# Kernel tuning notes

Hardware: AMD Instinct MI355X
Metric: run time of the kernel (lower is better)

Reference implementation:

```python
import jax, jax.numpy as jnp
import numpy as np

B, S, E, H = 8, 2048, 1024, 128  # batch, seq, emd_dim, head_size
DROP_P = 0.1


def setup_inputs() -> dict:
    key = jax.random.key(0)
    kx, ku, kq, kk, kv = jax.random.split(key, 5)
    x = jax.random.normal(kx, (B, S, E), dtype=jnp.float32)
    drop_u = jax.random.uniform(ku, (B, S, S), dtype=jnp.float32)
    # Linear(emd_dim, head_size, bias=False): store weights as [E, H] so y = x @ W
    scale = 1.0 / np.sqrt(E)
    wq = jax.random.uniform(kq, (E, H), dtype=jnp.float32, minval=-scale, maxval=scale)
    wk = jax.random.uniform(kk, (E, H), dtype=jnp.float32, minval=-scale, maxval=scale)
    wv = jax.random.uniform(kv, (E, H), dtype=jnp.float32, minval=-scale, maxval=scale)
    return {"x": x, "wq": wq, "wk": wk, "wv": wv, "drop_u": drop_u}


def reference(x, wq, wk, wv, drop_u):
    Edim = x.shape[-1]
    q = x @ wq  # [B,S,H]
    k = x @ wk
    v = x @ wv
    # NOTE: module scales by emd_dim**-0.5 (E), not head_size**-0.5
    att = jnp.einsum("bsh,bth->bst", q, k) * (Edim ** -0.5)
    att = jax.nn.softmax(att, axis=-1)
    # deterministic inverted dropout with p=0.1
    keep = (drop_u >= DROP_P).astype(att.dtype) / (1.0 - DROP_P)
    att = att * keep
    return jnp.einsum("bst,bth->bsh", att, v)
```

## Files before the change

### kernel.cpp

```cpp
#include <hip/hip_runtime.h>
#include <hip/hip_bf16.h>
#include <stdint.h>
#include <stddef.h>

#define B_ 8
#define S_ 2048
#define E_ 1024
#define H_ 128
#define NR_ (B_ * S_)

typedef __attribute__((ext_vector_type(8))) short short8;
typedef __attribute__((ext_vector_type(4))) short short4v;
typedef __attribute__((ext_vector_type(4))) float f32x4;

__device__ __forceinline__ short f2bf(float f){
  uint32_t u = __builtin_bit_cast(uint32_t, f);
  u = (u + 0x7FFFu + ((u >> 16) & 1u)) >> 16;
  return (short)(uint16_t)u;
}

__device__ __forceinline__ short8 pack8(f32x4 a, f32x4 b){
  union { short8 s; uint32_t u[4]; } r;
  asm("v_cvt_pk_bf16_f32 %0, %1, %2" : "=v"(r.u[0]) : "v"(a[0]), "v"(a[1]));
  asm("v_cvt_pk_bf16_f32 %0, %1, %2" : "=v"(r.u[1]) : "v"(a[2]), "v"(a[3]));
  asm("v_cvt_pk_bf16_f32 %0, %1, %2" : "=v"(r.u[2]) : "v"(b[0]), "v"(b[1]));
  asm("v_cvt_pk_bf16_f32 %0, %1, %2" : "=v"(r.u[3]) : "v"(b[2]), "v"(b[3]));
  return r.s;
}

#define GLOBAL_AS __attribute__((address_space(1)))
#define LDS_AS    __attribute__((address_space(3)))
__device__ __forceinline__ void async16(const void* g, void* l){
  __builtin_amdgcn_global_load_lds((const GLOBAL_AS uint32_t*)g,
                                   (LDS_AS uint32_t*)l, 16, 0, 0);
}

__global__ void prep(const float* __restrict__ wq, const float* __restrict__ wk,
                     const float* __restrict__ wv, short* __restrict__ wt){
  __shared__ float t[32][33];
  int idx = blockIdx.x;
  int hb  = idx & 3;
  int eb  = (idx >> 2) & 31;
  int w   = idx >> 7;
  const float* src = (w == 0) ? wq : (w == 1) ? wk : wv;
  int c  = threadIdx.x & 31;
  int r0 = threadIdx.x >> 5;
#pragma unroll
  for (int i = 0; i < 4; i++){
    int r = r0 * 4 + i;
    t[r][c] = src[(size_t)(eb * 32 + r) * H_ + hb * 32 + c];
  }
  __syncthreads();
#pragma unroll
  for (int i = 0; i < 4; i++){
    int r = r0 * 4 + i;
    wt[(size_t)(w * 128 + hb * 32 + r) * E_ + eb * 32 + c] = f2bf(t[c][r]);
  }
}

__launch_bounds__(256)
__global__ void qkv_gemm(const float* __restrict__ x, const short* __restrict__ wt,
                         short* __restrict__ qm, short* __restrict__ km,
                         short* __restrict__ vt){
  __shared__ __align__(16) short smem[16896];
  const int wave = threadIdx.x >> 6;
  const int lane = threadIdx.x & 63;
  const int l16  = lane & 15;
  const int quad = lane >> 4;
  const int nb   = blockIdx.x;
  const int m0   = blockIdx.y * 128;
  const int n0   = nb * 128;

  f32x4 acc[4][4];
#pragma unroll
  for (int i = 0; i < 4; i++)
#pragma unroll
    for (int j = 0; j < 4; j++) acc[i][j] = (f32x4)(0.0f);

  int cA[2], rA[2], qA[2];
#pragma unroll
  for (int i = 0; i < 2; i++){
    cA[i] = wave * 2 + i;
    rA[i] = cA[i] * 16 + (lane >> 2);
    qA[i] = ((lane & 3) ^ ((rA[i] >> 1) & 3)) & 3;
  }

  f32x4 a0[2], a1[2];

#define A_LOAD(k0)                                                            \
  {                                                                           \
    _Pragma("unroll")                                                         \
    for (int i = 0; i < 2; i++){                                              \
      const float* s_ = x + (size_t)(m0 + rA[i]) * E_ + (k0) + qA[i] * 8;     \
      a0[i] = *(const f32x4*)s_;                                              \
      a1[i] = *(const f32x4*)(s_ + 4);                                        \
    }                                                                         \
  }

#define A_WRITE(buf)                                                          \
  {                                                                           \
    _Pragma("unroll")                                                         \
    for (int i = 0; i < 2; i++)                                               \
      *(short8*)((char*)(smem + (buf) * 4096) + cA[i] * 1024 + lane * 16) =   \
          pack8(a0[i], a1[i]);                                                \
  }

#define B_STAGE(buf, k0)                                                      \
  {                                                                           \
    _Pragma("unroll")                                                         \
    for (int i = 0; i < 2; i++){                                              \
      int c = wave * 2 + i;                                                   \
      int r = c * 16 + (lane >> 2);                                           \
      int q = ((lane & 3) ^ ((r >> 1) & 3)) & 3;                              \
      async16(wt + (size_t)(n0 + r) * E_ + (k0) + q * 8,                      \
              (char*)(smem + 8192 + (buf) * 4096) + c * 1024);                \
    }                                                                         \
  }

  A_LOAD(0)
  B_STAGE(0, 0)
  A_WRITE(0)
  for (int ks = 0; ks < 32; ks++){
    const int k0 = ks * 32;
    __syncthreads();
    if (ks < 31){
      A_LOAD(k0 + 32)
      B_STAGE((ks + 1) & 1, k0 + 32)
    }

    const short* a = smem + (ks & 1) * 4096;
    const short* b = smem + 8192 + (ks & 1) * 4096;
    short8 af[4], bf[4];
#pragma unroll
    for (int t = 0; t < 4; t++){
      int ra = (wave & 1) * 64 + t * 16 + l16;
      int pa = (quad ^ ((ra >> 1) & 3)) & 3;
      af[t] = *(const short8*)(a + ra * 32 + pa * 8);
      int rb = (wave >> 1) * 64 + t * 16 + l16;
      int pb = (quad ^ ((rb >> 1) & 3)) & 3;
      bf[t] = *(const short8*)(b + rb * 32 + pb * 8);
    }
#pragma unroll
    for (int mt = 0; mt < 4; mt++)
#pragma unroll
      for (int nt = 0; nt < 4; nt++)
        acc[mt][nt] = __builtin_amdgcn_mfma_f32_16x16x32_bf16(af[mt], bf[nt], acc[mt][nt], 0, 0, 0);

    if (ks < 31){
      A_WRITE((ks + 1) & 1)
    }
  }
#undef A_LOAD
#undef A_WRITE
#undef B_STAGE

  if (nb != 2){
    short* dst = (nb == 0) ? qm : km;
#pragma unroll
    for (int mt = 0; mt < 4; mt++)
#pragma unroll
      for (int nt = 0; nt < 4; nt++){
        int row = m0 + (wave & 1) * 64 + mt * 16 + quad * 4;
        int col = (wave >> 1) * 64 + nt * 16 + l16;
#pragma unroll
        for (int r = 0; r < 4; r++)
          dst[(size_t)(row + r) * H_ + col] = f2bf(acc[mt][nt][r]);
      }
  } else {
    __syncthreads();
#pragma unroll
    for (int mt = 0; mt < 4; mt++)
#pragma unroll
      for (int nt = 0; nt < 4; nt++){
        int scol = (wave & 1) * 64 + mt * 16 + quad * 4;
        int hrow = (wave >> 1) * 64 + nt * 16 + l16;
        short4v t4;
#pragma unroll
        for (int r = 0; r < 4; r++) t4[r] = f2bf(acc[mt][nt][r]);
        *(short4v*)(smem + hrow * 132 + scol) = t4;
      }
    __syncthreads();
    int h   = threadIdx.x >> 1;
    int s0  = (threadIdx.x & 1) * 64;
    int bb_ = m0 >> 11;
    short* dstv = vt + ((size_t)bb_ * H_ + h) * S_ + (m0 & (S_ - 1)) + s0;
    const short* srcv = smem + h * 132 + s0;
#pragma unroll
    for (int i = 0; i < 8; i++)
      *(short8*)(dstv + i * 8) = *(const short8*)(srcv + i * 8);
  }
}

__launch_bounds__(512)
__global__ void attn(const short* __restrict__ qm, const short* __restrict__ km,
                     const short* __restrict__ vtm, const float* __restrict__ du,
                     float* __restrict__ po, float* __restrict__ pl,
                     float* __restrict__ out, int split){
  const int wave = threadIdx.x >> 6;
  const int lane = threadIdx.x & 63;
  const int l16  = lane & 15;
  const int quad = lane >> 4;
  const int sp   = blockIdx.x & (split - 1);
  const int rbk  = blockIdx.x / split;
  const int b    = rbk >> 4;
  const int m0   = (rbk & 15) * 128 + wave * 16;
  const int seg  = S_ / split;

  const short* qb  = qm  + ((size_t)b * S_ + m0) * H_;
  const short* kb  = km  + (size_t)b * S_ * H_;
  const short* vb  = vtm + (size_t)b * H_ * S_;
  const float* dub = du  + ((size_t)b * S_ + m0) * S_;

  __shared__ __align__(16) short kls[8192];
  __shared__ __align__(16) short vls[8192];
  __shared__ short pbuf[8][16][72];
  short* pb = &pbuf[wave][0][0];

  short8 qf[4];
#pragma unroll
  for (int kc = 0; kc < 4; kc++)
    qf[kc] = *(const short8*)(qb + (size_t)l16 * H_ + kc * 32 + quad * 8);

  f32x4 o[8];
#pragma unroll
  for (int ht = 0; ht < 8; ht++) o[ht] = (f32x4)(0.0f);
  float lpart[4] = {0.f, 0.f, 0.f, 0.f};

  const float SC2  = 0.045084220f;
  const float KINV = 1.0f / 0.9f;

  const int tbeg = sp * seg;
  for (int t0 = tbeg; t0 < tbeg + seg; t0 += 64){
#pragma unroll
    for (int i = 0; i < 2; i++){
      int c = wave * 2 + i;
      int r = c * 4 + (lane >> 4);
      int s = lane & 15;
      int q = (s & 8) | ((s ^ r) & 7);
      async16(kb + (size_t)(t0 + r) * H_ + q * 8, (char*)kls + c * 1024);
    }
#pragma unroll
    for (int i = 0; i < 2; i++){
      int c = wave * 2 + i;
      int r = c * 8 + (lane >> 3);
      int s = lane & 7;
      int q = (s ^ r) & 7;
      async16(vb + (size_t)r * S_ + t0 + q * 8, (char*)vls + c * 1024);
    }
    __syncthreads();

    const float* dp = dub + (size_t)l16 * S_ + t0 + quad * 8;
    f32x4 u0 = *(const f32x4*)(dp);
    f32x4 u1 = *(const f32x4*)(dp + 4);
    f32x4 u2 = *(const f32x4*)(dp + 32);
    f32x4 u3 = *(const f32x4*)(dp + 36);

    f32x4 s[4];
#pragma unroll
    for (int nt = 0; nt < 4; nt++) s[nt] = (f32x4)(0.0f);
#pragma unroll
    for (int nt = 0; nt < 4; nt++){
      int row = nt * 16 + l16;
#pragma unroll
      for (int kc = 0; kc < 4; kc++){
        int q  = kc * 4 + quad;
        int ph = (q & 8) | ((q ^ row) & 7);
        short8 bf = *(const short8*)((const char*)kls + row * 256 + ph * 16);
        s[nt] = __builtin_amdgcn_mfma_f32_16x16x32_bf16(qf[kc], bf, s[nt], 0, 0, 0);
      }
    }

#pragma unroll
    for (int nt = 0; nt < 4; nt++)
#pragma unroll
      for (int r = 0; r < 4; r++){
        float p = exp2f(s[nt][r] * SC2);
        lpart[r] += p;
        pb[(quad * 4 + r) * 72 + nt * 16 + l16] = f2bf(p);
      }

    __builtin_amdgcn_sched_barrier(0);
    __builtin_amdgcn_s_waitcnt(0xC07F);
    __builtin_amdgcn_sched_barrier(0);

    const short* pr = pb + l16 * 72 + quad * 8;
    short8 pb0 = *(const short8*)(pr);
    short8 pb1 = *(const short8*)(pr + 32);
    short8 pa0, pa1;
#pragma unroll
    for (int j = 0; j < 4; j++){
      pa0[j]     = (u0[j] >= 0.1f) ? pb0[j]     : (short)0;
      pa0[j + 4] = (u1[j] >= 0.1f) ? pb0[j + 4] : (short)0;
      pa1[j]     = (u2[j] >= 0.1f) ? pb1[j]     : (short)0;
      pa1[j + 4] = (u3[j] >= 0.1f) ? pb1[j + 4] : (short)0;
    }

#pragma unroll
    for (int ht = 0; ht < 8; ht++){
      int row = ht * 16 + l16;
#pragma unroll
      for (int half = 0; half < 2; half++){
        int q  = half * 4 + quad;
        int ph = (q ^ row) & 7;
        short8 vf = *(const short8*)((const char*)vls + row * 128 + ph * 16);
        o[ht] = __builtin_amdgcn_mfma_f32_16x16x32_bf16(half ? pa1 : pa0, vf, o[ht], 0, 0, 0);
      }
    }
    __syncthreads();
  }

  float lrow[4];
#pragma unroll
  for (int r = 0; r < 4; r++){
    float v = lpart[r];
    v += __shfl_xor(v, 1);
    v += __shfl_xor(v, 2);
    v += __shfl_xor(v, 4);
    v += __shfl_xor(v, 8);
    lrow[r] = v;
  }

  if (split == 1){
    float* op = out + ((size_t)b * S_ + m0) * H_;
#pragma unroll
    for (int ht = 0; ht < 8; ht++)
#pragma unroll
      for (int r = 0; r < 4; r++)
        op[(size_t)(quad * 4 + r) * H_ + ht * 16 + l16] = o[ht][r] * KINV / lrow[r];
  } else {
#pragma unroll
    for (int r = 0; r < 4; r++){
      size_t R = (size_t)b * S_ + m0 + quad * 4 + r;
#pragma unroll
      for (int ht = 0; ht < 8; ht++)
        po[((size_t)sp * NR_ + R) * H_ + ht * 16 + l16] = o[ht][r] * KINV;
      if (l16 == 0) pl[(size_t)sp * NR_ + R] = lrow[r];
    }
  }
}

__global__ void combine(const float* __restrict__ po, const float* __restrict__ pl,
                        float* __restrict__ out, int split){
  int row = blockIdx.x;
  int col = threadIdx.x;
  float num = 0.f, den = 0.f;
  for (int s = 0; s < split; s++){
    num += po[((size_t)s * NR_ + row) * H_ + col];
    den += pl[(size_t)s * NR_ + row];
  }
  out[(size_t)row * H_ + col] = num / den;
}

extern "C" void kernel_launch(void* const* d_in, const int* in_sizes, int n_in,
                              void* d_out, int out_size, void* d_ws, size_t ws_size,
                              hipStream_t stream){
  const float* x  = (const float*)d_in[0];
  const float* wq = (const float*)d_in[1];
  const float* wk = (const float*)d_in[2];
  const float* wv = (const float*)d_in[3];
  const float* du = (const float*)d_in[4];
  float* out = (float*)d_out;

  const size_t MiB = 1048576;
  char* ws = (char*)d_ws;
  short* qm = (short*)(ws);
  short* km = (short*)(ws + 4 * MiB);
  short* vt = (short*)(ws + 8 * MiB);
  short* wt = (short*)(ws + 44 * MiB);
  float* pl = (float*)(ws + 45 * MiB);
  float* po = (float*)(ws + 45 * MiB + 524288);

  size_t base  = 45 * MiB + 524288;
  size_t needA = base + 32 * MiB;
  size_t needB = base + 16 * MiB;
  int split = (ws_size >= needA) ? 4 : (ws_size >= needB) ? 2 : 1;

  hipLaunchKernelGGL(prep,     dim3(384),         dim3(256), 0, stream, wq, wk, wv, wt);
  hipLaunchKernelGGL(qkv_gemm, dim3(3, 128),      dim3(256), 0, stream, x, wt, qm, km, vt);
  hipLaunchKernelGGL(attn,     dim3(128 * split), dim3(512), 0, stream,
                     qm, km, vt, du, po, pl, out, split);
  if (split > 1)
    hipLaunchKernelGGL(combine, dim3(NR_), dim3(H_), 0, stream, po, pl, out, split);
}
```

Measured before the change: 293.3 us.

## Double-buffer K tiles in LDS to prefetch the next tile during compute

K tiles now live in two LDS buffers. The next iteration's K tile is loaded asynchronously while the current QK^T MFMAs run, and the barrier placement is reworked to match. The V load moves to just after the top-of-loop barrier, and a new barrier sits before the PV stage. The aim is to hide global-load latency behind compute. In exchange it uses 16 KB more LDS, which may cut occupancy. The mid-loop full vmcnt wait may also stall on the prefetch, and the last iteration issues one redundant prefetch.

```diff
diff --git a/kernel.cpp b/kernel.cpp
--- a/kernel.cpp
+++ b/kernel.cpp
@@ -211,7 +211,7 @@
   const short* vb  = vtm + (size_t)b * H_ * S_;
   const float* dub = du  + ((size_t)b * S_ + m0) * S_;
 
-  __shared__ __align__(16) short kls[8192];
+  __shared__ __align__(16) short kls[2][8192];
   __shared__ __align__(16) short vls[8192];
   __shared__ short pbuf[8][16][72];
   short* pb = &pbuf[wave][0][0];
@@ -229,16 +229,30 @@
   const float SC2  = 0.045084220f;
   const float KINV = 1.0f / 0.9f;
 
+#define K_STAGE(bufi, ts)                                                     \
+  {                                                                           \
+    _Pragma("unroll")                                                         \
+    for (int i = 0; i < 2; i++){                                              \
+      int c = wave * 2 + i;                                                   \
+      int r = c * 4 + (lane >> 4);                                            \
+      int s = lane & 15;                                                      \
+      int q = (s & 8) | ((s ^ r) & 7);                                        \
+      async16(kb + (size_t)((ts) + r) * H_ + q * 8,                           \
+              (char*)kls + (bufi) * 16384 + c * 1024);                        \
+    }                                                                         \
+  }
+
   const int tbeg = sp * seg;
-  for (int t0 = tbeg; t0 < tbeg + seg; t0 += 64){
-#pragma unroll
-    for (int i = 0; i < 2; i++){
-      int c = wave * 2 + i;
-      int r = c * 4 + (lane >> 4);
-      int s = lane & 15;
-      int q = (s & 8) | ((s ^ r) & 7);
-      async16(kb + (size_t)(t0 + r) * H_ + q * 8, (char*)kls + c * 1024);
-    }
+  const int nIt  = seg >> 6;
+
+  K_STAGE(0, tbeg)
+
+  for (int it = 0; it < nIt; ++it){
+    const int t0  = tbeg + (it << 6);
+    const int cur = it & 1;
+
+    __syncthreads();
+
 #pragma unroll
     for (int i = 0; i < 2; i++){
       int c = wave * 2 + i;
@@ -247,7 +261,6 @@
       int q = (s ^ r) & 7;
       async16(vb + (size_t)r * S_ + t0 + q * 8, (char*)vls + c * 1024);
     }
-    __syncthreads();
 
     const float* dp = dub + (size_t)l16 * S_ + t0 + quad * 8;
     f32x4 u0 = *(const f32x4*)(dp);
@@ -255,6 +268,9 @@
     f32x4 u2 = *(const f32x4*)(dp + 32);
     f32x4 u3 = *(const f32x4*)(dp + 36);
 
+    const int nt0 = (it + 1 < nIt) ? (t0 + 64) : tbeg;
+    K_STAGE(cur ^ 1, nt0)
+
     f32x4 s[4];
 #pragma unroll
     for (int nt = 0; nt < 4; nt++) s[nt] = (f32x4)(0.0f);
@@ -265,7 +281,7 @@
       for (int kc = 0; kc < 4; kc++){
         int q  = kc * 4 + quad;
         int ph = (q & 8) | ((q ^ row) & 7);
-        short8 bf = *(const short8*)((const char*)kls + row * 256 + ph * 16);
+        short8 bf = *(const short8*)((const char*)kls + cur * 16384 + row * 256 + ph * 16);
         s[nt] = __builtin_amdgcn_mfma_f32_16x16x32_bf16(qf[kc], bf, s[nt], 0, 0, 0);
       }
     }
@@ -294,6 +310,8 @@
       pa1[j]     = (u2[j] >= 0.1f) ? pb1[j]     : (short)0;
       pa1[j + 4] = (u3[j] >= 0.1f) ? pb1[j + 4] : (short)0;
     }
+
+    __syncthreads();
 
 #pragma unroll
     for (int ht = 0; ht < 8; ht++){
@@ -306,8 +324,8 @@
         o[ht] = __builtin_amdgcn_mfma_f32_16x16x32_bf16(half ? pa1 : pa0, vf, o[ht], 0, 0, 0);
       }
     }
-    __syncthreads();
-  }
+  }
+#undef K_STAGE
 
   float lrow[4];
 #pragma unroll
```

Result: no change. 290.2 us (-1.1%).
